# Optimization experiments

Hardware: AMD Instinct MI355X
Metric: run time of the kernel (lower is better)

The kernel has to match this reference:

```python
import jax, jax.numpy as jnp
import numpy as np

B, N, C = 16, 1024, 256
SIZE = (512, 640)          # (H, W) image size
STRIDE = 8
H0, W0 = SIZE[0] // STRIDE, SIZE[1] // STRIDE   # 64, 80
P_TOK = H0 * W0                                  # 5120 base tokens
NHEAD, NLVL, NPTS = 8, 4, 4
HD = C // NHEAD
NUM_CLASSES = 7


def setup_inputs() -> dict:
    key = jax.random.key(0)
    ks = jax.random.split(key, 16)
    g = lambda k, shape, s=0.02: jax.random.normal(k, shape, jnp.float32) * s
    return {
        "q_t": jax.random.normal(ks[0], (B, N, C), jnp.float32),
        "h_t": jax.random.normal(ks[1], (B, P_TOK, C), jnp.float32),
        "p_head_t": jax.random.uniform(ks[2], (B, N, 2), jnp.float32)
                    * jnp.array([SIZE[1], SIZE[0]], jnp.float32),  # (x,y) in image coords
        "W_off": g(ks[3], (C, NHEAD * NLVL * NPTS * 2)),
        "b_off": g(ks[4], (NHEAD * NLVL * NPTS * 2,)),
        "W_attn": g(ks[5], (C, NHEAD * NLVL * NPTS)),
        "b_attn": g(ks[6], (NHEAD * NLVL * NPTS,)),
        "W_v": g(ks[7], (C, C)), "b_v": g(ks[8], (C,)),
        "W_o": g(ks[9], (C, C)), "b_o": g(ks[10], (C,)),
        "W_p1": g(ks[11], (2 * C, C)), "b_p1": g(ks[12], (C,)),
        "W_p2": g(ks[13], (C, NUM_CLASSES)), "b_p2": g(ks[14], (NUM_CLASSES,)),
    }


def _bilinear_sample(value_l, loc):
    """value_l: (B,Hl,Wl,nh,hd); loc: (B,N,nh,NPTS,2) in [0,1] normalized (x,y).
    grid_sample semantics: align_corners=False, padding_mode='zeros'.
    Returns (B,nh,N,NPTS,hd)."""
    Bb, Hl, Wl = value_l.shape[0], value_l.shape[1], value_l.shape[2]
    x = loc[..., 0] * Wl - 0.5
    y = loc[..., 1] * Hl - 0.5
    x0 = jnp.floor(x); y0 = jnp.floor(y)
    wx = x - x0; wy = y - y0
    x0i = x0.astype(jnp.int32); y0i = y0.astype(jnp.int32)
    flat = value_l.reshape(Bb, Hl * Wl, NHEAD, HD).transpose(0, 2, 1, 3)  # (B,nh,S,hd)

    def corner(xi, yi):
        valid = ((xi >= 0) & (xi < Wl) & (yi >= 0) & (yi < Hl)).astype(value_l.dtype)
        idx = (jnp.clip(yi, 0, Hl - 1) * Wl + jnp.clip(xi, 0, Wl - 1)).transpose(0, 2, 1, 3)  # (B,nh,N,P)
        g = jnp.take_along_axis(flat, idx.reshape(Bb, NHEAD, -1)[..., None], axis=2)
        g = g.reshape(Bb, NHEAD, idx.shape[2], idx.shape[3], HD)
        return g * valid.transpose(0, 2, 1, 3)[..., None]

    tw = lambda w: w.transpose(0, 2, 1, 3)[..., None]  # (B,nh,N,P,1)
    return (corner(x0i, y0i) * tw((1 - wx) * (1 - wy))
            + corner(x0i + 1, y0i) * tw(wx * (1 - wy))
            + corner(x0i, y0i + 1) * tw((1 - wx) * wy)
            + corner(x0i + 1, y0i + 1) * tw(wx * wy))


def reference(q_t, h_t, p_head_t, W_off, b_off, W_attn, b_attn,
              W_v, b_v, W_o, b_o, W_p1, b_p1, W_p2, b_p2):
    # normalize point predictions to [0,1] (x by W, y by H)
    p_norm = jnp.clip(p_head_t / jnp.array([SIZE[1], SIZE[0]], jnp.float32), 0.0, 1.0)

    # ---- get_deformable_inputs: 4-level pyramid by 2x2 average pooling ----
    cur = h_t.reshape(B, H0, W0, C)
    feats, shapes = [], []
    for l in range(NLVL):
        feats.append(cur)
        shapes.append((cur.shape[1], cur.shape[2]))
        if l < NLVL - 1:
            h, w = cur.shape[1], cur.shape[2]
            cur = cur.reshape(B, h // 2, 2, w // 2, 2, C).mean(axis=(2, 4))
    f_scales = jnp.concatenate([f.reshape(B, -1, C) for f in feats], axis=1)  # (B,S,C)

    # ---- DMSMHA_Block (multi-scale deformable attention) ----
    value = (f_scales @ W_v + b_v).reshape(B, -1, NHEAD, HD)
    offsets = (q_t @ W_off + b_off).reshape(B, N, NHEAD, NLVL, NPTS, 2)
    attn = jax.nn.softmax(
        (q_t @ W_attn + b_attn).reshape(B, N, NHEAD, NLVL * NPTS), axis=-1
    ).reshape(B, N, NHEAD, NLVL, NPTS)

    out = jnp.zeros((B, NHEAD, N, HD), jnp.float32)
    start = 0
    for l, (Hl, Wl) in enumerate(shapes):
        Sl = Hl * Wl
        vl = value[:, start:start + Sl].reshape(B, Hl, Wl, NHEAD, HD)
        start += Sl
        norm = jnp.array([Wl, Hl], jnp.float32)
        loc = p_norm[:, :, None, None, :] + offsets[:, :, :, l] / norm  # (B,N,nh,P,2)
        sampled = _bilinear_sample(vl, loc)                              # (B,nh,N,P,hd)
        w = attn[:, :, :, l].transpose(0, 2, 1, 3)                       # (B,nh,N,P)
        out = out + jnp.einsum('bhnp,bhnpd->bhnd', w, sampled)

    q_local = out.transpose(0, 2, 1, 3).reshape(B, N, C) @ W_o + b_o

    # ---- fuse + MLP head ----
    q_fused = jnp.concatenate([q_t, q_local], axis=-1)
    hid = jax.nn.relu(q_fused @ W_p1 + b_p1)
    logits = hid @ W_p2 + b_p2   # (B,N,num_classes)
    return logits
```

## Files before the change

### kernel.cpp

```cpp
#include <hip/hip_runtime.h>
#include <math.h>


namespace {

constexpr int kB = 16;
constexpr int kN = 1024;
constexpr int kC = 256;
constexpr int kNCLS = 7;
constexpr int kSTOT = 6800;

typedef __attribute__((ext_vector_type(8))) short short8;
typedef __attribute__((ext_vector_type(4))) float f32x4;

__device__ inline ushort f2bf(float f) {
  union { float f; unsigned u; } v; v.f = f;
  unsigned r = (v.u + 0x7fffu + ((v.u >> 16) & 1u)) >> 16;
  return (ushort)r;
}
__device__ inline float bf2f(ushort h) {
  union { unsigned u; float f; } v; v.u = ((unsigned)h) << 16;
  return v.f;
}

__device__ inline void gload16(const ushort* g, ushort* l) {
  __builtin_amdgcn_global_load_lds(
      (const __attribute__((address_space(1))) void*)g,
      (__attribute__((address_space(3))) void*)l, 16, 0, 0);
}

__global__ void cast_f2b_kernel(const float* __restrict__ in, ushort* __restrict__ out, int n4) {
  int i = blockIdx.x * 256 + threadIdx.x;
  if (i >= n4) return;
  float4 v = ((const float4*)in)[i];
  ((ushort4*)out)[i] = make_ushort4(f2bf(v.x), f2bf(v.y), f2bf(v.z), f2bf(v.w));
}

__global__ void pool_b2b_kernel(const ushort* __restrict__ fin, ushort* __restrict__ fout,
                                int oh, int ow, int so_in, int so_out) {
  int idx = blockIdx.x * 256 + threadIdx.x;
  if (idx >= kB * oh * ow * kC) return;
  int c = idx & 255; int t = idx >> 8;
  int x = t % ow; t /= ow; int y = t % oh; int b = t / oh;
  int iw = ow * 2;
  const ushort* p = fin + (((size_t)b * kSTOT + so_in + y * 2 * iw + x * 2) << 8) + c;
  float s = 0.25f * (bf2f(p[0]) + bf2f(p[256]) + bf2f(p[iw * 256]) + bf2f(p[iw * 256 + 256]));
  fout[(((size_t)b * kSTOT + so_out + y * ow + x) << 8) + c] = f2bf(s);
}

__global__ void wtrans_all_kernel(const float* __restrict__ s0, const float* __restrict__ s1,
                                  const float* __restrict__ s2, const float* __restrict__ s3,
                                  const float* __restrict__ s4,
                                  ushort* __restrict__ d0, ushort* __restrict__ d1,
                                  ushort* __restrict__ d2, ushort* __restrict__ d3,
                                  ushort* __restrict__ d4) {
  __shared__ float t[32][33];
  const float* W; ushort* Wt; int K, N;
  switch (blockIdx.z) {
    case 0: W = s0; Wt = d0; K = 256; N = 256; break;
    case 1: W = s1; Wt = d1; K = 256; N = 256; break;
    case 2: W = s2; Wt = d2; K = 256; N = 128; break;
    case 3: W = s3; Wt = d3; K = 256; N = 256; break;
    default: W = s4; Wt = d4; K = 512; N = 256; break;
  }
  int nx = blockIdx.x << 5, ky = blockIdx.y << 5;
  if (nx >= N || ky >= K) return;
  int lx = threadIdx.x & 31, ly = threadIdx.x >> 5;
#pragma unroll
  for (int i = 0; i < 32; i += 8)
    t[ly + i][lx] = W[(size_t)(ky + ly + i) * N + nx + lx];
  __syncthreads();
#pragma unroll
  for (int i = 0; i < 32; i += 8)
    Wt[(size_t)(nx + ly + i) * K + ky + lx] = f2bf(t[lx][ly + i]);
}

template <int KTOT, bool SPLITK, int OMODE, bool RELU>
__global__ __launch_bounds__(256) void gemm_bf16_kernel(
    const ushort* __restrict__ A, const ushort* __restrict__ A2,
    const ushort* __restrict__ Wt, const float* __restrict__ bias,
    const float* __restrict__ bias2, void* __restrict__ Cout,
    void* __restrict__ Cout2, int ldc) {
  __shared__ ushort Asm[2][128 * 32];
  __shared__ ushort Bsm[2][128 * 32];
  const int tid = threadIdx.x;
  const int w = tid >> 6, l = tid & 63;
  const int bm = blockIdx.y << 7, bn = blockIdx.x << 7;
  const int wm = w >> 1, wn = w & 1;

  const int c0 = w * 2, c1 = w * 2 + 1;
  const int G0 = c0 * 64 + l, G1 = c1 * 64 + l;
  const int r0 = G0 >> 2, g0 = G0 & 3;
  const int r1 = G1 >> 2, g1 = G1 & 3;
  const int sz0 = (g0 ^ ((r0 >> 1) & 3)) << 3;
  const int sz1 = (g1 ^ ((r1 >> 1) & 3)) << 3;
  const int ak = SPLITK ? 256 : KTOT;
  const ushort* sA0 = A + (size_t)(bm + r0) * ak + sz0;
  const ushort* sA1 = A + (size_t)(bm + r1) * ak + sz1;
  const ushort* sA0b = SPLITK ? A2 + (size_t)(bm + r0) * 256 + sz0 : nullptr;
  const ushort* sA1b = SPLITK ? A2 + (size_t)(bm + r1) * 256 + sz1 : nullptr;
  const ushort* sB0 = Wt + (size_t)(bn + r0) * KTOT + sz0;
  const ushort* sB1 = Wt + (size_t)(bn + r1) * KTOT + sz1;

  const int e = l >> 4, rl = l & 15;
  int aoff[4], boff[4];
#pragma unroll
  for (int i = 0; i < 4; ++i) {
    int r = wm * 64 + i * 16 + rl;
    aoff[i] = r * 32 + ((e ^ ((r >> 1) & 3)) << 3);
    int rb = wn * 64 + i * 16 + rl;
    boff[i] = rb * 32 + ((e ^ ((rb >> 1) & 3)) << 3);
  }

  f32x4 acc[4][4];
#pragma unroll
  for (int i = 0; i < 4; ++i)
#pragma unroll
    for (int j = 0; j < 4; ++j) acc[i][j] = (f32x4){0.f, 0.f, 0.f, 0.f};

  auto stage = [&](int buf, int k0) {
    const ushort *a0, *a1;
    if (SPLITK && k0 >= 256) {
      a0 = sA0b + (k0 - 256);
      a1 = sA1b + (k0 - 256);
    } else {
      a0 = sA0 + k0;
      a1 = sA1 + k0;
    }
    gload16(a0, &Asm[buf][c0 * 512]);
    gload16(a1, &Asm[buf][c1 * 512]);
    gload16(sB0 + k0, &Bsm[buf][c0 * 512]);
    gload16(sB1 + k0, &Bsm[buf][c1 * 512]);
  };

  constexpr int nt = KTOT / 32;
  stage(0, 0);
  __syncthreads();
  for (int t = 0; t < nt; ++t) {
    const int cur = t & 1;
    if (t + 1 < nt) stage(cur ^ 1, (t + 1) * 32);
    short8 af[4], bfr[4];
#pragma unroll
    for (int i = 0; i < 4; ++i) af[i] = *(const short8*)&Asm[cur][aoff[i]];
#pragma unroll
    for (int j = 0; j < 4; ++j) bfr[j] = *(const short8*)&Bsm[cur][boff[j]];
#pragma unroll
    for (int i = 0; i < 4; ++i)
#pragma unroll
      for (int j = 0; j < 4; ++j)
        acc[i][j] = __builtin_amdgcn_mfma_f32_16x16x32_bf16(bfr[j], af[i], acc[i][j], 0, 0, 0);
    __syncthreads();
  }

#pragma unroll
  for (int j = 0; j < 4; ++j) {
    int ch = bn + wn * 64 + j * 16 + e * 4;
    float4 b4;
    if (OMODE == 2)
      b4 = (ch < 256) ? *(const float4*)(bias + ch) : *(const float4*)(bias2 + ch - 256);
    else
      b4 = *(const float4*)(bias + ch);
    float bv[4] = {b4.x, b4.y, b4.z, b4.w};
#pragma unroll
    for (int i = 0; i < 4; ++i) {
      int sp = bm + wm * 64 + i * 16 + rl;
      float v[4];
#pragma unroll
      for (int r = 0; r < 4; ++r) {
        v[r] = acc[i][j][r] + bv[r];
        if (RELU) v[r] = fmaxf(v[r], 0.f);
      }
      if (OMODE == 0) {
        *(float4*)&((float*)Cout)[(size_t)sp * ldc + ch] = make_float4(v[0], v[1], v[2], v[3]);
      } else if (OMODE == 1) {
        *(ushort4*)&((ushort*)Cout)[(size_t)sp * ldc + ch] =
            make_ushort4(f2bf(v[0]), f2bf(v[1]), f2bf(v[2]), f2bf(v[3]));
      } else {
        if (ch < 256)
          *(float4*)&((float*)Cout)[(size_t)sp * 256 + ch] = make_float4(v[0], v[1], v[2], v[3]);
        else
          *(float4*)&((float*)Cout2)[(size_t)sp * 128 + (ch - 256)] =
              make_float4(v[0], v[1], v[2], v[3]);
      }
    }
  }
}

__global__ __launch_bounds__(256) void gemm_f32a_kernel(
    const float* __restrict__ A, const ushort* __restrict__ Wt,
    const float* __restrict__ bias, ushort* __restrict__ Cout) {
  __shared__ ushort Asm[2][128 * 32];
  __shared__ ushort Bsm[2][128 * 32];
  const int tid = threadIdx.x;
  const int w = tid >> 6, l = tid & 63;
  const int by = blockIdx.y;
  const int bn = blockIdx.x << 7;
  const int bm = by << 7;
  const int wm = w >> 1, wn = w & 1;

  const int ar = tid >> 1, ah = tid & 1;
  const float* aSrc = A + (size_t)(bm + ar) * 256 + ah * 16;
  const int s_ar = (ar >> 1) & 3;
  const int ad0 = ar * 32 + (((2 * ah + 0) ^ s_ar) << 3);
  const int ad1 = ar * 32 + (((2 * ah + 1) ^ s_ar) << 3);

  const int c0 = w * 2, c1 = w * 2 + 1;
  const int G0 = c0 * 64 + l, G1 = c1 * 64 + l;
  const int r0 = G0 >> 2, g0 = G0 & 3;
  const int r1 = G1 >> 2, g1 = G1 & 3;
  const ushort* sB0 = Wt + (size_t)(bn + r0) * 256 + ((g0 ^ ((r0 >> 1) & 3)) << 3);
  const ushort* sB1 = Wt + (size_t)(bn + r1) * 256 + ((g1 ^ ((r1 >> 1) & 3)) << 3);

  const int e = l >> 4, rl = l & 15;
  int aoff[4], boff[4];
#pragma unroll
  for (int i = 0; i < 4; ++i) {
    int r = wm * 64 + i * 16 + rl;
    aoff[i] = r * 32 + ((e ^ ((r >> 1) & 3)) << 3);
    int rb = wn * 64 + i * 16 + rl;
    boff[i] = rb * 32 + ((e ^ ((rb >> 1) & 3)) << 3);
  }

  f32x4 acc[4][4];
#pragma unroll
  for (int i = 0; i < 4; ++i)
#pragma unroll
    for (int j = 0; j < 4; ++j) acc[i][j] = (f32x4){0.f, 0.f, 0.f, 0.f};

  float4 av[4];
  auto loadA = [&](int k0) {
#pragma unroll
    for (int q = 0; q < 4; ++q) av[q] = *(const float4*)(aSrc + k0 + 4 * q);
  };
  auto writeA = [&](int buf) {
    ushort u[16];
#pragma unroll
    for (int q = 0; q < 4; ++q) {
      u[4 * q + 0] = f2bf(av[q].x);
      u[4 * q + 1] = f2bf(av[q].y);
      u[4 * q + 2] = f2bf(av[q].z);
      u[4 * q + 3] = f2bf(av[q].w);
    }
    *(short8*)&Asm[buf][ad0] =
        (short8){(short)u[0], (short)u[1], (short)u[2], (short)u[3],
                 (short)u[4], (short)u[5], (short)u[6], (short)u[7]};
    *(short8*)&Asm[buf][ad1] =
        (short8){(short)u[8], (short)u[9], (short)u[10], (short)u[11],
                 (short)u[12], (short)u[13], (short)u[14], (short)u[15]};
  };
  auto stageB = [&](int buf, int k0) {
    gload16(sB0 + k0, &Bsm[buf][c0 * 512]);
    gload16(sB1 + k0, &Bsm[buf][c1 * 512]);
  };

  loadA(0);
  stageB(0, 0);
  writeA(0);
  __syncthreads();
  for (int t = 0; t < 8; ++t) {
    const int cur = t & 1;
    if (t < 7) {
      loadA((t + 1) * 32);
      stageB(cur ^ 1, (t + 1) * 32);
    }
    short8 af[4], bfr[4];
#pragma unroll
    for (int i = 0; i < 4; ++i) af[i] = *(const short8*)&Asm[cur][aoff[i]];
#pragma unroll
    for (int j = 0; j < 4; ++j) bfr[j] = *(const short8*)&Bsm[cur][boff[j]];
#pragma unroll
    for (int i = 0; i < 4; ++i)
#pragma unroll
      for (int j = 0; j < 4; ++j)
        acc[i][j] = __builtin_amdgcn_mfma_f32_16x16x32_bf16(bfr[j], af[i], acc[i][j], 0, 0, 0);
    if (t < 7) writeA(cur ^ 1);
    __syncthreads();
  }

  const int b = by / 40;
  const int sb = (by - b * 40) << 7;
  ushort* outB = Cout + (((size_t)(b * 6800 + sb)) << 8);
#pragma unroll
  for (int j = 0; j < 4; ++j) {
    int ch = bn + wn * 64 + j * 16 + e * 4;
    float4 b4 = *(const float4*)(bias + ch);
    float bv[4] = {b4.x, b4.y, b4.z, b4.w};
#pragma unroll
    for (int i = 0; i < 4; ++i) {
      int sp = wm * 64 + i * 16 + rl;
      float v[4];
#pragma unroll
      for (int r = 0; r < 4; ++r) v[r] = acc[i][j][r] + bv[r];
      *(ushort4*)&outB[(size_t)sp * 256 + ch] =
          make_ushort4(f2bf(v[0]), f2bf(v[1]), f2bf(v[2]), f2bf(v[3]));
    }
  }
}

__global__ void deform_kernel(
    const ushort* __restrict__ value, const float* __restrict__ off,
    const float* __restrict__ attnl, const float* __restrict__ p_head,
    ushort* __restrict__ samp) {
  int blk = (int)blockIdx.x;
  int sw = (blk & 7) * 256 + (blk >> 3);
  int wvi = (sw << 2) + (threadIdx.x >> 6);
  int l = threadIdx.x & 63;
  int nq = l >> 5;
  int lh = l & 31;
  int h = lh >> 2;
  int pt = wvi * 2 + nq;
  int b = pt >> 10;
  size_t bn = (size_t)pt;

  float ph = (lh < 2) ? p_head[bn * 2 + lh] : 0.f;
  float px = __shfl(ph, (nq << 5) + 0, 64) * (1.0f / 640.0f);
  float py = __shfl(ph, (nq << 5) + 1, 64) * (1.0f / 512.0f);
  px = fminf(fmaxf(px, 0.f), 1.f);
  py = fminf(fmaxf(py, 0.f), 1.f);

  const float4* offp = (const float4*)(off + (bn << 8));
  float4 ofv0 = offp[2 * lh];
  float4 ofv1 = offp[2 * lh + 1];
  float4 atv = ((const float4*)(attnl + (bn << 7)))[lh];

  float m = fmaxf(fmaxf(atv.x, atv.y), fmaxf(atv.z, atv.w));
  m = fmaxf(m, __shfl_xor(m, 1, 64));
  m = fmaxf(m, __shfl_xor(m, 2, 64));
  float e0 = expf(atv.x - m), e1 = expf(atv.y - m);
  float e2 = expf(atv.z - m), e3 = expf(atv.w - m);
  float s = e0 + e1 + e2 + e3;
  s += __shfl_xor(s, 1, 64);
  s += __shfl_xor(s, 2, 64);
  float inv = 1.f / s;
  atv = make_float4(e0 * inv, e1 * inv, e2 * inv, e3 * inv);

  float acc[8];
#pragma unroll
  for (int i = 0; i < 8; ++i) acc[i] = 0.f;
  const ushort* vbb = value + (((size_t)b * kSTOT) << 8) + (lh << 3);

#pragma unroll 1
  for (int lv = 0; lv < 4; ++lv) {
    const int Wl = 80 >> lv, Hl = 64 >> lv;
    const int offL = (lv == 0) ? 0 : (lv == 1) ? 5120 : (lv == 2) ? 6400 : 6720;
    const ushort* vb = vbb + (((size_t)offL) << 8);
    const int src = (nq << 5) + (h << 2) + lv;
    const float fx = px * (float)Wl - 0.5f;
    const float fy = py * (float)Hl - 0.5f;
#pragma unroll
    for (int pp = 0; pp < 4; ++pp) {
      float sx, sy;
      if ((pp >> 1) == 0) {
        sx = (pp & 1) ? ofv0.z : ofv0.x;
        sy = (pp & 1) ? ofv0.w : ofv0.y;
      } else {
        sx = (pp & 1) ? ofv1.z : ofv1.x;
        sy = (pp & 1) ? ofv1.w : ofv1.y;
      }
      float ox = __shfl(sx, src, 64);
      float oy = __shfl(sy, src, 64);
      float sa = pp == 0 ? atv.x : pp == 1 ? atv.y : pp == 2 ? atv.z : atv.w;
      float aw = __shfl(sa, src, 64);

      float xx = fx + ox;
      float yy = fy + oy;
      float x0f = floorf(xx), y0f = floorf(yy);
      float wx = xx - x0f, wy = yy - y0f;
      int x0 = (int)x0f, y0 = (int)y0f;
      float w00 = (1.f - wx) * (1.f - wy) * aw;
      float w01 = wx * (1.f - wy) * aw;
      float w10 = (1.f - wx) * wy * aw;
      float w11 = wx * wy * aw;
      auto corner = [&](int xi, int yi, float wgt) {
        bool valid = (xi >= 0) && (xi < Wl) && (yi >= 0) && (yi < Hl);
        int xc = xi < 0 ? 0 : (xi > Wl - 1 ? Wl - 1 : xi);
        int yc = yi < 0 ? 0 : (yi > Hl - 1 ? Hl - 1 : yi);
        short8 d = *(const short8*)(vb + (((size_t)(yc * Wl + xc)) << 8));
        float wg = valid ? wgt : 0.f;
#pragma unroll
        for (int i = 0; i < 8; ++i) acc[i] = fmaf(wg, bf2f((ushort)d[i]), acc[i]);
      };
      corner(x0, y0, w00);
      corner(x0 + 1, y0, w01);
      corner(x0, y0 + 1, w10);
      corner(x0 + 1, y0 + 1, w11);
    }
  }
  ushort o[8];
#pragma unroll
  for (int i = 0; i < 8; ++i) o[i] = f2bf(acc[i]);
  *(short8*)(samp + (bn << 8) + (lh << 3)) =
      (short8){(short)o[0], (short)o[1], (short)o[2], (short)o[3],
               (short)o[4], (short)o[5], (short)o[6], (short)o[7]};
}

__global__ void head_kernel(const float* __restrict__ hid, const float* __restrict__ W2,
                            const float* __restrict__ b2, float* __restrict__ outp) {
  int gid = blockIdx.x * 256 + threadIdx.x;
  int wave = gid >> 6;
  int lane = threadIdx.x & 63;
  if (wave >= kB * kN) return;
  const float* hrow = hid + ((size_t)wave << 8);
  float acc[kNCLS];
#pragma unroll
  for (int j = 0; j < kNCLS; ++j) acc[j] = 0.f;
  for (int k = lane; k < kC; k += 64) {
    float hv = hrow[k];
    const float* wr = W2 + k * kNCLS;
#pragma unroll
    for (int j = 0; j < kNCLS; ++j) acc[j] = fmaf(hv, wr[j], acc[j]);
  }
#pragma unroll
  for (int m = 32; m > 0; m >>= 1) {
#pragma unroll
    for (int j = 0; j < kNCLS; ++j) acc[j] += __shfl_xor(acc[j], m);
  }
  float r = 0.f;
#pragma unroll
  for (int j = 0; j < kNCLS; ++j)
    if (lane == j) r = acc[j] + b2[j];
  if (lane < kNCLS) outp[(size_t)wave * kNCLS + lane] = r;
}

}

extern "C" void kernel_launch(void* const* d_in, const int* in_sizes, int n_in,
                              void* d_out, int out_size, void* d_ws, size_t ws_size,
                              hipStream_t stream) {
  const float* q_t    = (const float*)d_in[0];
  const float* h_t    = (const float*)d_in[1];
  const float* p_head = (const float*)d_in[2];
  const float* W_off  = (const float*)d_in[3];
  const float* b_off  = (const float*)d_in[4];
  const float* W_attn = (const float*)d_in[5];
  const float* b_attn = (const float*)d_in[6];
  const float* W_v    = (const float*)d_in[7];
  const float* b_v    = (const float*)d_in[8];
  const float* W_o    = (const float*)d_in[9];
  const float* b_o    = (const float*)d_in[10];
  const float* W_p1   = (const float*)d_in[11];
  const float* b_p1   = (const float*)d_in[12];
  const float* W_p2   = (const float*)d_in[13];
  const float* b_p2   = (const float*)d_in[14];
  float* out = (float*)d_out;
  char* wsb = (char*)d_ws;

  ushort* value = (ushort*)(wsb + 55705600);
  ushort* q_bf  = (ushort*)(wsb + 111411200);
  float*  offb  = (float*)(wsb + 119799808);
  float*  attnl = (float*)(wsb + 136577024);
  ushort* samp  = (ushort*)(wsb + 144965632);
  ushort* qloc  = (ushort*)(wsb + 153354240);
  float*  hid   = (float*)(wsb + 161742848);
  ushort* wtp   = (ushort*)(wsb + 178520064);
  ushort* Wt_v  = wtp;
  ushort* Wt_oa = wtp + 65536;
  ushort* Wt_o  = wtp + 163840;
  ushort* Wt_p1 = wtp + 229376;

  cast_f2b_kernel<<<4096, 256, 0, stream>>>(q_t, q_bf, kB * kN * 64);

  wtrans_all_kernel<<<dim3(8, 16, 5), 256, 0, stream>>>(
      W_v, W_off, W_attn, W_o, W_p1,
      Wt_v, Wt_oa, Wt_oa + 65536, Wt_o, Wt_p1);

  gemm_f32a_kernel<<<dim3(2, 640), 256, 0, stream>>>(h_t, Wt_v, b_v, value);

  pool_b2b_kernel<<<20480, 256, 0, stream>>>(value, value, 32, 40, 0, 5120);
  pool_b2b_kernel<<<5120, 256, 0, stream>>>(value, value, 16, 20, 5120, 6400);
  pool_b2b_kernel<<<1280, 256, 0, stream>>>(value, value, 8, 10, 6400, 6720);

  gemm_bf16_kernel<256, false, 2, false><<<dim3(3, 128), 256, 0, stream>>>(
      q_bf, nullptr, Wt_oa, b_off, b_attn, offb, attnl, 256);

  deform_kernel<<<2048, 256, 0, stream>>>(value, offb, attnl, p_head, samp);

  gemm_bf16_kernel<256, false, 1, false><<<dim3(2, 128), 256, 0, stream>>>(
      samp, nullptr, Wt_o, b_o, nullptr, qloc, nullptr, 256);

  gemm_bf16_kernel<512, true, 0, true><<<dim3(2, 128), 256, 0, stream>>>(
      q_bf, qloc, Wt_p1, b_p1, nullptr, hid, nullptr, 256);

  head_kernel<<<4096, 256, 0, stream>>>(hid, W_p2, b_p2, out);
}
```

Baseline: 152.1 us.

## Fold output projection W_o into first MLP layer weights

Precomputes W_o @ W_p1[256:] and the folded bias b_o @ W_p1[256:] + b_p1 in a small per-call kernel. The sampled deformable-attention output then feeds straight into the MLP GEMM, which removes the separate W_o GEMM and its qloc intermediate. The combined weight is rounded to bf16 once, which slightly changes numerics compared with two chained bf16 GEMMs. It also adds a small serial dot-product kernel that recomputes the folded weights on every call.

```diff
diff --git a/kernel.cpp b/kernel.cpp
--- a/kernel.cpp
+++ b/kernel.cpp
@@ -73,6 +73,30 @@
 #pragma unroll
   for (int i = 0; i < 32; i += 8)
     Wt[(size_t)(nx + ly + i) * K + ky + lx] = f2bf(t[lx][ly + i]);
+}
+
+__global__ void wcomb_kernel(const float* __restrict__ W_o, const float* __restrict__ W_p1,
+                             const float* __restrict__ b_o, const float* __restrict__ b_p1,
+                             const ushort* __restrict__ Wt_p1,
+                             ushort* __restrict__ Wt_p1c, float* __restrict__ bp1c) {
+  __shared__ float wcol[256];
+  __shared__ float wsum[4];
+  int h = blockIdx.x;
+  int in = threadIdx.x;
+  wcol[in] = W_p1[(size_t)(256 + in) * 256 + h];
+  __syncthreads();
+  float s = 0.f;
+  const float* wo = W_o + (size_t)in * 256;
+#pragma unroll 4
+  for (int out = 0; out < 256; ++out) s = fmaf(wo[out], wcol[out], s);
+  Wt_p1c[(size_t)h * 512 + 256 + in] = f2bf(s);
+  Wt_p1c[(size_t)h * 512 + in] = Wt_p1[(size_t)h * 512 + in];
+  float part = b_o[in] * wcol[in];
+#pragma unroll
+  for (int m = 32; m > 0; m >>= 1) part += __shfl_xor(part, m);
+  if ((in & 63) == 0) wsum[in >> 6] = part;
+  __syncthreads();
+  if (in == 0) bp1c[h] = b_p1[h] + wsum[0] + wsum[1] + wsum[2] + wsum[3];
 }
 
 template <int KTOT, bool SPLITK, int OMODE, bool RELU>
@@ -450,13 +474,14 @@
   float*  offb  = (float*)(wsb + 119799808);
   float*  attnl = (float*)(wsb + 136577024);
   ushort* samp  = (ushort*)(wsb + 144965632);
-  ushort* qloc  = (ushort*)(wsb + 153354240);
   float*  hid   = (float*)(wsb + 161742848);
   ushort* wtp   = (ushort*)(wsb + 178520064);
-  ushort* Wt_v  = wtp;
-  ushort* Wt_oa = wtp + 65536;
-  ushort* Wt_o  = wtp + 163840;
-  ushort* Wt_p1 = wtp + 229376;
+  ushort* Wt_v   = wtp;
+  ushort* Wt_oa  = wtp + 65536;
+  ushort* Wt_o   = wtp + 163840;
+  ushort* Wt_p1  = wtp + 229376;
+  ushort* Wt_p1c = wtp + 360448;
+  float*  bp1c   = (float*)(wtp + 491520);
 
   cast_f2b_kernel<<<4096, 256, 0, stream>>>(q_t, q_bf, kB * kN * 64);
 
@@ -464,6 +489,8 @@
       W_v, W_off, W_attn, W_o, W_p1,
       Wt_v, Wt_oa, Wt_oa + 65536, Wt_o, Wt_p1);
 
+  wcomb_kernel<<<256, 256, 0, stream>>>(W_o, W_p1, b_o, b_p1, Wt_p1, Wt_p1c, bp1c);
+
   gemm_f32a_kernel<<<dim3(2, 640), 256, 0, stream>>>(h_t, Wt_v, b_v, value);
 
   pool_b2b_kernel<<<20480, 256, 0, stream>>>(value, value, 32, 40, 0, 5120);
@@ -475,11 +502,8 @@
 
   deform_kernel<<<2048, 256, 0, stream>>>(value, offb, attnl, p_head, samp);
 
-  gemm_bf16_kernel<256, false, 1, false><<<dim3(2, 128), 256, 0, stream>>>(
-      samp, nullptr, Wt_o, b_o, nullptr, qloc, nullptr, 256);
-
   gemm_bf16_kernel<512, true, 0, true><<<dim3(2, 128), 256, 0, stream>>>(
-      q_bf, qloc, Wt_p1, b_p1, nullptr, hid, nullptr, 256);
+      q_bf, samp, Wt_p1c, bp1c, nullptr, hid, nullptr, 256);
 
   head_kernel<<<4096, 256, 0, stream>>>(hid, W_p2, b_p2, out);
 }
```

Result: slower. 155.2 us (+2.0%).
